# Kernel tuning notes

Hardware: AMD Instinct MI355X
Metric: run time of the kernel (lower is better)

Reference implementation:

```python
import jax, jax.numpy as jnp
import numpy as np

# Grid / filter configuration (matches init_kwargs)
NLAT_IN, NLON_IN = 361, 720
NLAT_OUT, NLON_OUT = 361, 720
K = 9                       # kernel_size for piecewise-linear basis, kernel_shape=[3,4]
PSCALE = NLON_IN // NLON_OUT  # longitude stride between output longitudes
NNZ = 65536
B, CIN, COUT = 2, 64, 64


def setup_inputs() -> dict:
    key = jax.random.key(0)
    k0, k1, k2, k3, k4, k5 = jax.random.split(key, 6)
    x = jax.random.normal(k0, (B, CIN, NLAT_IN, NLON_IN), dtype=jnp.float32)
    psi_ker_idx = jax.random.randint(k1, (NNZ,), 0, K)
    psi_row_idx = jax.random.randint(k2, (NNZ,), 0, NLAT_OUT)
    psi_col_idx = jax.random.randint(k3, (NNZ,), 0, NLAT_IN * NLON_IN)
    # quadrature-merged, normalized basis values are small positive numbers
    psi_vals = jax.random.uniform(k4, (NNZ,), dtype=jnp.float32) / K
    scale = (1.0 / (CIN * K)) ** 0.5
    weight = scale * jax.random.normal(k5, (COUT, CIN, K), dtype=jnp.float32)
    bias = jnp.zeros((COUT,), dtype=jnp.float32)
    return {
        "x": x,
        "psi_vals": psi_vals,
        "weight": weight,
        "bias": bias,
        "psi_ker_idx": psi_ker_idx,
        "psi_row_idx": psi_row_idx,
        "psi_col_idx": psi_col_idx,
    }


def reference(x, psi_vals, weight, bias, psi_ker_idx, psi_row_idx, psi_col_idx):
    """DISCO S2 conv: y[b,c,k,lo,p] = sum_nz psi_vals * x[b,c,lat_in, (lon_in+p*PSCALE)%NLON_IN]
    restricted to nz with ker==k, row==lo; then channel mixing with weight (COUT,CIN,K) + bias.
    Matches torch fallback which rolls x by PSCALE per output longitude and does sparse bmm."""
    b, c, nlat_in, nlon_in = x.shape
    lat_in = psi_col_idx // nlon_in          # (nnz,)
    lon_in = psi_col_idx % nlon_in           # (nnz,)
    seg = psi_ker_idx * NLAT_OUT + psi_row_idx  # (nnz,) segment id over (K, nlat_out)
    xf = x.reshape(b * c, nlat_in, nlon_in)

    def step(carry, p):
        lon = (lon_in + p * PSCALE) % nlon_in        # rolled longitude index, (nnz,)
        g = xf[:, lat_in, lon]                       # (BC, nnz) gather
        contrib = (psi_vals * g).T                   # (nnz, BC)
        yk = jax.ops.segment_sum(contrib, seg, num_segments=K * NLAT_OUT)  # (K*nlat_out, BC)
        y = yk.reshape(K, NLAT_OUT, b, c)
        o = jnp.einsum("klbc,ock->bol", y, weight)   # (B, COUT, nlat_out)
        return carry, o

    _, ys = jax.lax.scan(step, None, jnp.arange(NLON_OUT))  # (nlon_out, B, COUT, nlat_out)
    out = jnp.moveaxis(ys, 0, -1)                            # (B, COUT, nlat_out, nlon_out)
    return out + bias[None, :, None, None]
```

## Files before the change

### kernel.cpp

```cpp
#include <hip/hip_runtime.h>

typedef unsigned int uint;
typedef unsigned short ushort;

#define NLAT 361
#define NLON 720
#define NNZT 65536
#define CIN 64
#define COUT 64
#define NK 9
#define PADL 784
#define ROWCAP 384
#define CKTOT 576
#define YPS 168
#define WTS 640
#define XROWB (16*PADL*8)

typedef __attribute__((ext_vector_type(8))) short short8v;
typedef __attribute__((ext_vector_type(4))) float f32x4;

__device__ __forceinline__ float bfu(uint u){ return __uint_as_float(u<<16); }
__device__ __forceinline__ float bfh(uint u){ return __uint_as_float(u & 0xffff0000u); }
__device__ __forceinline__ ushort f2bf(float f){
  uint b = __float_as_uint(f);
  return (ushort)((b + 0x7fffu + ((b>>16)&1u)) >> 16);
}
__device__ __forceinline__ uint packbf2(float f0, float f1){
  uint b0 = __float_as_uint(f0), b1 = __float_as_uint(f1);
  uint r0 = (b0 + 0x7fffu + ((b0>>16)&1u)) >> 16;
  uint r1 = ((b1 + 0x7fffu + ((b1>>16)&1u)) >> 16) << 16;
  return r0 | r1;
}

__global__ __launch_bounds__(256) void k_csr(const int* __restrict__ ker, const int* __restrict__ row,
                                             const int* __restrict__ col, const float* __restrict__ vals,
                                             int2* __restrict__ meta_g, int* __restrict__ kptr_g){
  const int lo = blockIdx.x, tid = threadIdx.x;
  __shared__ int cnt2[256*NK];
  #pragma unroll
  for (int kk=0;kk<NK;kk++) cnt2[tid*NK+kk]=0;
  __syncthreads();
  for (int i=tid;i<NNZT;i+=256) if (row[i]==lo) cnt2[tid*NK + ker[i]]++;
  __syncthreads();
  if (tid==0){
    int run=0;
    for (int kk=0;kk<NK;kk++){
      kptr_g[lo*10+kk]=run;
      for (int t=0;t<256;t++){ int tmp=cnt2[t*NK+kk]; cnt2[t*NK+kk]=run; run+=tmp; }
    }
    kptr_g[lo*10+9]=run;
  }
  __syncthreads();
  for (int i=tid;i<NNZT;i+=256) if (row[i]==lo){
    int kk=ker[i];
    int off=cnt2[tid*NK+kk]++;
    if (off<ROWCAP){
      int c=col[i];
      int lat=c/NLON, lon=c-lat*NLON;
      uint vb = __float_as_uint(vals[i]) & 0xfffffc00u;
      meta_g[lo*ROWCAP+off]=make_int2(lat*XROWB + lon*8, (int)(vb | (uint)lon));
    }
  }
}

__global__ __launch_bounds__(256) void k_xb(const float* __restrict__ x, ushort* __restrict__ xb){
  const int bid=blockIdx.x, tid=threadIdx.x;
  const int b=bid/NLAT, lat=bid-b*NLAT;
  const float* xs = x + (size_t)b*CIN*NLAT*NLON + (size_t)lat*NLON;
  ushort* xd = xb + (size_t)(b*NLAT+lat)*16*PADL*4;
  const size_t S=(size_t)NLAT*NLON;
  for (int idx=tid; idx<16*PADL; idx+=256){
    int cq=idx/PADL, j=idx-cq*PADL;
    int jj = (j<NLON)? j : j-NLON;
    const float* xc = xs + (size_t)(cq*4)*S + jj;
    uint lo32 = packbf2(xc[0], xc[S]);
    uint hi32 = packbf2(xc[2*S], xc[3*S]);
    *(uint2*)(xd + (size_t)(cq*PADL + j)*4) = make_uint2(lo32, hi32);
  }
}

__global__ __launch_bounds__(256) void k_wt(const float* __restrict__ w, ushort* __restrict__ wt){
  int idx = blockIdx.x*256 + threadIdx.x;
  if (idx >= COUT*WTS) return;
  int oc = idx/WTS, ckl = idx-oc*WTS;
  int chunk = ckl/160, q = ckl-chunk*160;
  ushort v = 0;
  if (q < 144){
    int wvq=q/36, r=q-wvq*36;
    int kk=r>>2, j=r&3;
    v = f2bf(w[oc*CKTOT + (chunk*16 + wvq*4 + j)*NK + kk]);
  }
  wt[oc*WTS + ckl] = v;
}

template<int USE_XB>
__global__ __launch_bounds__(256,4) void k_main(const float* __restrict__ x, const ushort* __restrict__ xb,
    const int2* __restrict__ meta_g, const int* __restrict__ kptr_g,
    const ushort* __restrict__ wt, const float* __restrict__ bias, float* __restrict__ out){
  const int bid=blockIdx.x, tid=threadIdx.x;
  const int lo=bid/6; const int rem=bid-lo*6;
  const int b=rem/3, pq=rem-(rem/3)*3;

  __shared__ int2 meta[ROWCAP];
  __shared__ __align__(16) ushort Yp[64*YPS];

  int kp[10];
  #pragma unroll
  for (int kk=0;kk<10;kk++){ int v=kptr_g[lo*10+kk]; kp[kk]=v<ROWCAP?v:ROWCAP; }
  for (int i=tid;i<kp[9];i+=256) meta[i]=meta_g[lo*ROWCAP+i];
  for (int idx=tid; idx<64*8; idx+=256){
    int p=idx>>3, j=idx&7;
    *(uint*)((char*)Yp + p*(YPS*2) + 288 + j*4) = 0;
  }
  __syncthreads();

  const int lane=tid&63, wv=tid>>6;
  const int wvu = __builtin_amdgcn_readfirstlane(wv);
  const int l15=lane&15, kg=lane>>4;
  const char* xb8 = (const char*)xb + (size_t)b*NLAT*(size_t)XROWB;
  const char* wtb = (const char*)wt + ((wv*16+l15)*WTS + kg*8)*2;
  const char* ypb = (const char*)Yp + l15*(YPS*2) + kg*16;
  char* ydst = (char*)Yp + lane*(YPS*2) + wv*72;

  float b4[4];
  #pragma unroll
  for (int r=0;r<4;r++) b4[r]=bias[wv*16 + kg*4 + r];

#define GADDR(M) ((uint)(M).x + lanep8 + (((((uint)(M).y)&0x3ffu) >= thr) ? (uint)-5760 : 0u))
#define GVAL(M)  __uint_as_float(((uint)(M).y) & 0xfffffc00u)
#define GCONS(U,V,ACC,AI) { ACC[0][AI]+=(V)*bfu((U).x); ACC[1][AI]+=(V)*bfh((U).x); \
                            ACC[2][AI]+=(V)*bfu((U).y); ACC[3][AI]+=(V)*bfh((U).y); }
#define GB1F(M,ACC,AI) { \
      uint lon=((uint)(M).y)&0x3ffu; float v=GVAL(M); \
      int lat=(int)(((uint)(M).x)/(uint)XROWB); \
      int s=(int)lon+p0; s=(s>=NLON)?s-NLON:s; \
      int widx=s+lane; widx=(widx>=NLON)?widx-NLON:widx; \
      int base=((b*CIN + chunk*16 + wv*4)*NLAT + lat)*NLON + widx; \
      ACC[0][AI]+=v*x[base]; ACC[1][AI]+=v*x[base+NLAT*NLON]; \
      ACC[2][AI]+=v*x[base+2*NLAT*NLON]; ACC[3][AI]+=v*x[base+3*NLAT*NLON]; }

#define GSEG(ACC,KI,AI) { \
      int i=kp[KI]; const int e=kp[(KI)+1]; \
      if (USE_XB){ \
        for (; i+7<e; i+=8){ \
          int2 m0=meta[i],m1=meta[i+1],m2=meta[i+2],m3=meta[i+3]; \
          int2 m4=meta[i+4],m5=meta[i+5],m6=meta[i+6],m7=meta[i+7]; \
          uint2 u0=*(const uint2*)(xbase+GADDR(m0)); uint2 u1=*(const uint2*)(xbase+GADDR(m1)); \
          uint2 u2=*(const uint2*)(xbase+GADDR(m2)); uint2 u3=*(const uint2*)(xbase+GADDR(m3)); \
          uint2 u4=*(const uint2*)(xbase+GADDR(m4)); uint2 u5=*(const uint2*)(xbase+GADDR(m5)); \
          uint2 u6=*(const uint2*)(xbase+GADDR(m6)); uint2 u7=*(const uint2*)(xbase+GADDR(m7)); \
          GCONS(u0,GVAL(m0),ACC,AI); GCONS(u1,GVAL(m1),ACC,AI); \
          GCONS(u2,GVAL(m2),ACC,AI); GCONS(u3,GVAL(m3),ACC,AI); \
          GCONS(u4,GVAL(m4),ACC,AI); GCONS(u5,GVAL(m5),ACC,AI); \
          GCONS(u6,GVAL(m6),ACC,AI); GCONS(u7,GVAL(m7),ACC,AI); \
        } \
        for (; i+3<e; i+=4){ \
          int2 m0=meta[i],m1=meta[i+1],m2=meta[i+2],m3=meta[i+3]; \
          uint2 u0=*(const uint2*)(xbase+GADDR(m0)); uint2 u1=*(const uint2*)(xbase+GADDR(m1)); \
          uint2 u2=*(const uint2*)(xbase+GADDR(m2)); uint2 u3=*(const uint2*)(xbase+GADDR(m3)); \
          GCONS(u0,GVAL(m0),ACC,AI); GCONS(u1,GVAL(m1),ACC,AI); \
          GCONS(u2,GVAL(m2),ACC,AI); GCONS(u3,GVAL(m3),ACC,AI); \
        } \
        for (; i<e; i++){ int2 m0=meta[i]; \
          uint2 u0=*(const uint2*)(xbase+GADDR(m0)); GCONS(u0,GVAL(m0),ACC,AI); } \
      } else { \
        for (; i<e; i++){ int2 m0=meta[i]; GB1F(m0,ACC,AI); } \
      } }

  for (int pt=0;pt<4;pt++){
    const int p0 = pq*240 + pt*64;
    const uint thr = (uint)(NLON - p0);
    const uint lanep8 = (uint)(lane + p0)*8u;
    f32x4 outacc[4];
    #pragma unroll
    for (int c2=0;c2<4;c2++) outacc[c2]=(f32x4)0.f;

    for (int chunk=0;chunk<4;chunk++){
      short8v af[5];
      #pragma unroll
      for (int ks=0;ks<5;ks++)
        af[ks] = *(const short8v*)(wtb + (chunk*160 + ks*32)*2);

      const char* xbase = xb8 + (size_t)(chunk*4+wvu)*(PADL*8);

      {
        float acc1[4][5];
        #pragma unroll
        for (int j=0;j<4;j++)
          #pragma unroll
          for (int kk=0;kk<5;kk++) acc1[j][kk]=0.f;
        GSEG(acc1,0,0) GSEG(acc1,1,1) GSEG(acc1,2,2) GSEG(acc1,3,3) GSEG(acc1,4,4)
        __syncthreads();
        #pragma unroll
        for (int kk=0;kk<5;kk++){
          *(uint*)(ydst + (kk*4+0)*2) = packbf2(acc1[0][kk], acc1[1][kk]);
          *(uint*)(ydst + (kk*4+2)*2) = packbf2(acc1[2][kk], acc1[3][kk]);
        }
      }
      {
        float acc2[4][4];
        #pragma unroll
        for (int j=0;j<4;j++)
          #pragma unroll
          for (int kk=0;kk<4;kk++) acc2[j][kk]=0.f;
        GSEG(acc2,5,0) GSEG(acc2,6,1) GSEG(acc2,7,2) GSEG(acc2,8,3)
        #pragma unroll
        for (int kk=0;kk<4;kk++){
          *(uint*)(ydst + ((kk+5)*4+0)*2) = packbf2(acc2[0][kk], acc2[1][kk]);
          *(uint*)(ydst + ((kk+5)*4+2)*2) = packbf2(acc2[2][kk], acc2[3][kk]);
        }
      }
      __syncthreads();
      #pragma unroll
      for (int ptile=0;ptile<4;ptile++){
        #pragma unroll
        for (int ks=0;ks<5;ks++){
          short8v bf = *(const short8v*)(ypb + ptile*(16*YPS*2) + ks*64);
          outacc[ptile] = __builtin_amdgcn_mfma_f32_16x16x32_bf16(af[ks], bf, outacc[ptile], 0, 0, 0);
        }
      }
    }
    #pragma unroll
    for (int ptile=0;ptile<4;ptile++){
      const int pidx = pt*64 + ptile*16;
      if (pidx < 240){
        #pragma unroll
        for (int r=0;r<4;r++){
          int oc = wv*16 + kg*4 + r;
          int p  = pq*240 + pidx + l15;
          out[((size_t)(b*COUT+oc)*NLAT + lo)*NLON + p] = outacc[ptile][r] + b4[r];
        }
      }
    }
  }
}

extern "C" void kernel_launch(void* const* d_in, const int* in_sizes, int n_in,
                              void* d_out, int out_size, void* d_ws, size_t ws_size,
                              hipStream_t stream){
  const float* x   =(const float*)d_in[0];
  const float* vals=(const float*)d_in[1];
  const float* w   =(const float*)d_in[2];
  const float* bias=(const float*)d_in[3];
  const int* ker=(const int*)d_in[4];
  const int* row=(const int*)d_in[5];
  const int* col=(const int*)d_in[6];
  float* out=(float*)d_out;

  const size_t META_B=(size_t)NLAT*ROWCAP*sizeof(int2);
  const size_t KPTR_B=((size_t)NLAT*10*sizeof(int)+15)&~(size_t)15;
  const size_t WT_B=((size_t)COUT*WTS*sizeof(ushort)+15)&~(size_t)15;
  const size_t XB_B=(size_t)2*NLAT*16*PADL*4*sizeof(ushort);
  int2* meta_g=(int2*)d_ws;
  int*  kptr_g=(int*)((char*)d_ws+META_B);
  ushort* wt=(ushort*)((char*)d_ws+META_B+KPTR_B);
  ushort* xb=(ushort*)((char*)d_ws+META_B+KPTR_B+WT_B);
  const bool use_xb = ws_size >= META_B+KPTR_B+WT_B+XB_B;

  k_csr<<<dim3(NLAT), dim3(256), 0, stream>>>(ker,row,col,vals,meta_g,kptr_g);
  k_wt <<<dim3((COUT*WTS+255)/256), dim3(256), 0, stream>>>(w, wt);
  if (use_xb){
    k_xb<<<dim3(2*NLAT), dim3(256), 0, stream>>>(x, xb);
    k_main<1><<<dim3(NLAT*6), dim3(256), 0, stream>>>(x,xb,meta_g,kptr_g,wt,bias,out);
  } else {
    k_main<0><<<dim3(NLAT*6), dim3(256), 0, stream>>>(x,xb,meta_g,kptr_g,wt,bias,out);
  }
}
```

Baseline: 2.256 ms.

## Swap chunk/pt loop order, remap blocks per XCD, mask idle lanes in last tile

Loop order changes to chunk outer and pt inner. Each wave then reuses the same 4-channel slice of the bf16 x buffer across all four longitude tiles while it is cache-hot, keeping 16 MFMA accumulators live. The block index is remapped so consecutive logical blocks (same output latitude) land on the same XCD, for L2 locality of the shared meta/x rows. Lanes beyond the 240 longitudes in the last tile skip their gathers. The costs are higher register pressure from 64 accumulator floats with launch bounds of 4 blocks per CU, and weight fragments reloaded from global per MFMA.

```diff
diff --git a/kernel.cpp b/kernel.cpp
--- a/kernel.cpp
+++ b/kernel.cpp
@@ -97,7 +97,11 @@
 __global__ __launch_bounds__(256,4) void k_main(const float* __restrict__ x, const ushort* __restrict__ xb,
     const int2* __restrict__ meta_g, const int* __restrict__ kptr_g,
     const ushort* __restrict__ wt, const float* __restrict__ bias, float* __restrict__ out){
-  const int bid=blockIdx.x, tid=threadIdx.x;
+  const int nwg = NLAT*6;
+  const int qq = nwg/8, rr = nwg%8;
+  const int xcd = blockIdx.x & 7, sidx = blockIdx.x >> 3;
+  const int bid = (xcd<rr ? xcd*(qq+1) : rr*(qq+1) + (xcd-rr)*qq) + sidx;
+  const int tid=threadIdx.x;
   const int lo=bid/6; const int rem=bid-lo*6;
   const int b=rem/3, pq=rem-(rem/3)*3;
 
@@ -121,10 +125,6 @@
   const char* wtb = (const char*)wt + ((wv*16+l15)*WTS + kg*8)*2;
   const char* ypb = (const char*)Yp + l15*(YPS*2) + kg*16;
   char* ydst = (char*)Yp + lane*(YPS*2) + wv*72;
-
-  float b4[4];
-  #pragma unroll
-  for (int r=0;r<4;r++) b4[r]=bias[wv*16 + kg*4 + r];
 
 #define GADDR(M) ((uint)(M).x + lanep8 + (((((uint)(M).y)&0x3ffu) >= thr) ? (uint)-5760 : 0u))
 #define GVAL(M)  __uint_as_float(((uint)(M).y) & 0xfffffc00u)
@@ -167,21 +167,20 @@
         for (; i<e; i++){ int2 m0=meta[i]; GB1F(m0,ACC,AI); } \
       } }
 
-  for (int pt=0;pt<4;pt++){
-    const int p0 = pq*240 + pt*64;
-    const uint thr = (uint)(NLON - p0);
-    const uint lanep8 = (uint)(lane + p0)*8u;
-    f32x4 outacc[4];
+  f32x4 outacc[4][4];
+  #pragma unroll
+  for (int a=0;a<4;a++)
     #pragma unroll
-    for (int c2=0;c2<4;c2++) outacc[c2]=(f32x4)0.f;
-
-    for (int chunk=0;chunk<4;chunk++){
-      short8v af[5];
-      #pragma unroll
-      for (int ks=0;ks<5;ks++)
-        af[ks] = *(const short8v*)(wtb + (chunk*160 + ks*32)*2);
-
-      const char* xbase = xb8 + (size_t)(chunk*4+wvu)*(PADL*8);
+    for (int c2=0;c2<4;c2++) outacc[a][c2]=(f32x4)0.f;
+
+  for (int chunk=0;chunk<4;chunk++){
+    const char* xbase = xb8 + (size_t)(chunk*4+wvu)*(PADL*8);
+    #pragma unroll
+    for (int pt=0;pt<4;pt++){
+      const int p0 = pq*240 + pt*64;
+      const uint thr = (uint)(NLON - p0);
+      const uint lanep8 = (uint)(lane + p0)*8u;
+      const bool act = (pt<3) || (lane<48);
 
       {
         float acc1[4][5];
@@ -189,12 +188,14 @@
         for (int j=0;j<4;j++)
           #pragma unroll
           for (int kk=0;kk<5;kk++) acc1[j][kk]=0.f;
-        GSEG(acc1,0,0) GSEG(acc1,1,1) GSEG(acc1,2,2) GSEG(acc1,3,3) GSEG(acc1,4,4)
+        if (act){ GSEG(acc1,0,0) GSEG(acc1,1,1) GSEG(acc1,2,2) GSEG(acc1,3,3) GSEG(acc1,4,4) }
         __syncthreads();
-        #pragma unroll
-        for (int kk=0;kk<5;kk++){
-          *(uint*)(ydst + (kk*4+0)*2) = packbf2(acc1[0][kk], acc1[1][kk]);
-          *(uint*)(ydst + (kk*4+2)*2) = packbf2(acc1[2][kk], acc1[3][kk]);
+        if (act){
+          #pragma unroll
+          for (int kk=0;kk<5;kk++){
+            *(uint*)(ydst + (kk*4+0)*2) = packbf2(acc1[0][kk], acc1[1][kk]);
+            *(uint*)(ydst + (kk*4+2)*2) = packbf2(acc1[2][kk], acc1[3][kk]);
+          }
         }
       }
       {
@@ -203,11 +204,13 @@
         for (int j=0;j<4;j++)
           #pragma unroll
           for (int kk=0;kk<4;kk++) acc2[j][kk]=0.f;
-        GSEG(acc2,5,0) GSEG(acc2,6,1) GSEG(acc2,7,2) GSEG(acc2,8,3)
-        #pragma unroll
-        for (int kk=0;kk<4;kk++){
-          *(uint*)(ydst + ((kk+5)*4+0)*2) = packbf2(acc2[0][kk], acc2[1][kk]);
-          *(uint*)(ydst + ((kk+5)*4+2)*2) = packbf2(acc2[2][kk], acc2[3][kk]);
+        if (act){
+          GSEG(acc2,5,0) GSEG(acc2,6,1) GSEG(acc2,7,2) GSEG(acc2,8,3)
+          #pragma unroll
+          for (int kk=0;kk<4;kk++){
+            *(uint*)(ydst + ((kk+5)*4+0)*2) = packbf2(acc2[0][kk], acc2[1][kk]);
+            *(uint*)(ydst + ((kk+5)*4+2)*2) = packbf2(acc2[2][kk], acc2[3][kk]);
+          }
         }
       }
       __syncthreads();
@@ -216,10 +219,14 @@
         #pragma unroll
         for (int ks=0;ks<5;ks++){
           short8v bf = *(const short8v*)(ypb + ptile*(16*YPS*2) + ks*64);
-          outacc[ptile] = __builtin_amdgcn_mfma_f32_16x16x32_bf16(af[ks], bf, outacc[ptile], 0, 0, 0);
-        }
-      }
-    }
+          short8v afk = *(const short8v*)(wtb + (chunk*160 + ks*32)*2);
+          outacc[pt][ptile] = __builtin_amdgcn_mfma_f32_16x16x32_bf16(afk, bf, outacc[pt][ptile], 0, 0, 0);
+        }
+      }
+    }
+  }
+  #pragma unroll
+  for (int pt=0;pt<4;pt++)
     #pragma unroll
     for (int ptile=0;ptile<4;ptile++){
       const int pidx = pt*64 + ptile*16;
@@ -228,11 +235,10 @@
         for (int r=0;r<4;r++){
           int oc = wv*16 + kg*4 + r;
           int p  = pq*240 + pidx + l15;
-          out[((size_t)(b*COUT+oc)*NLAT + lo)*NLON + p] = outacc[ptile][r] + b4[r];
-        }
-      }
-    }
-  }
+          out[((size_t)(b*COUT+oc)*NLAT + lo)*NLON + p] = outacc[pt][ptile][r] + bias[oc];
+        }
+      }
+    }
 }
 
 extern "C" void kernel_launch(void* const* d_in, const int* in_sizes, int n_in,
```

Result: faster. 2.127 ms (-5.7%).

## Sort row nonzeros by gather address and dispatch kernel index per entry

Applied to the files above, without the earlier changes.

The CSR build no longer buckets nonzeros by kernel index. It packs the kernel index into the metadata word and rank-sorts each row's entries by gather address, so consecutive gathers touch nearby memory. The main loop then walks one flat list and uses a wave-uniform switch to pick the accumulator. It also skips gathers for inactive lanes in the last partial tile and reloads weight fragments per MFMA instead of holding them in registers. The switch per entry and the 9-wide accumulator add branching and register pressure, and the mantissa of the stored value is truncated further to make room for the index.

```diff
diff --git a/kernel.cpp b/kernel.cpp
--- a/kernel.cpp
+++ b/kernel.cpp
@@ -36,31 +36,35 @@
                                              const int* __restrict__ col, const float* __restrict__ vals,
                                              int2* __restrict__ meta_g, int* __restrict__ kptr_g){
   const int lo = blockIdx.x, tid = threadIdx.x;
-  __shared__ int cnt2[256*NK];
-  #pragma unroll
-  for (int kk=0;kk<NK;kk++) cnt2[tid*NK+kk]=0;
-  __syncthreads();
-  for (int i=tid;i<NNZT;i+=256) if (row[i]==lo) cnt2[tid*NK + ker[i]]++;
-  __syncthreads();
-  if (tid==0){
-    int run=0;
-    for (int kk=0;kk<NK;kk++){
-      kptr_g[lo*10+kk]=run;
-      for (int t=0;t<256;t++){ int tmp=cnt2[t*NK+kk]; cnt2[t*NK+kk]=run; run+=tmp; }
-    }
-    kptr_g[lo*10+9]=run;
-  }
-  __syncthreads();
+  __shared__ int cnt[256];
+  __shared__ int2 list[ROWCAP];
+  __shared__ int ntot;
+  int c=0;
+  for (int i=tid;i<NNZT;i+=256) if (row[i]==lo) c++;
+  cnt[tid]=c;
+  __syncthreads();
+  if (tid==0){ int run=0; for (int t=0;t<256;t++){ int tmp=cnt[t]; cnt[t]=run; run+=tmp; } ntot=run; }
+  __syncthreads();
+  int off=cnt[tid];
   for (int i=tid;i<NNZT;i+=256) if (row[i]==lo){
-    int kk=ker[i];
-    int off=cnt2[tid*NK+kk]++;
     if (off<ROWCAP){
-      int c=col[i];
-      int lat=c/NLON, lon=c-lat*NLON;
-      uint vb = __float_as_uint(vals[i]) & 0xfffffc00u;
-      meta_g[lo*ROWCAP+off]=make_int2(lat*XROWB + lon*8, (int)(vb | (uint)lon));
-    }
-  }
+      int cc=col[i]; int lat=cc/NLON, lon=cc-lat*NLON;
+      uint vb=__float_as_uint(vals[i])&0xffffc000u;
+      list[off]=make_int2(lat*XROWB+lon*8, (int)(vb|((uint)ker[i]<<10)|(uint)lon));
+    }
+    off++;
+  }
+  __syncthreads();
+  int n = ntot; if (n>ROWCAP) n=ROWCAP;
+  for (int i=tid;i<n;i+=256){
+    uint xi=(uint)list[i].x; int r=0;
+    for (int j=0;j<n;j++){
+      uint xj=(uint)list[j].x;
+      r += (xj<xi) || (xj==xi && j<i);
+    }
+    meta_g[lo*ROWCAP+r]=list[i];
+  }
+  if (tid==0) kptr_g[lo]=n;
 }
 
 __global__ __launch_bounds__(256) void k_xb(const float* __restrict__ x, ushort* __restrict__ xb){
@@ -104,110 +108,92 @@
   __shared__ int2 meta[ROWCAP];
   __shared__ __align__(16) ushort Yp[64*YPS];
 
-  int kp[10];
-  #pragma unroll
-  for (int kk=0;kk<10;kk++){ int v=kptr_g[lo*10+kk]; kp[kk]=v<ROWCAP?v:ROWCAP; }
-  for (int i=tid;i<kp[9];i+=256) meta[i]=meta_g[lo*ROWCAP+i];
+  int n = kptr_g[lo]; if (n>ROWCAP) n=ROWCAP;
+  for (int i=tid;i<n;i+=256) meta[i]=meta_g[lo*ROWCAP+i];
   for (int idx=tid; idx<64*8; idx+=256){
     int p=idx>>3, j=idx&7;
-    *(uint*)((char*)Yp + p*(YPS*2) + 288 + j*4) = 0;
-  }
-  __syncthreads();
-
-  const int lane=tid&63, wv=tid>>6;
+    *(uint*)((char*)Yp + p*(YPS*2) + 288 + j*4)=0;
+  }
+  __syncthreads();
+
+  const int lane=tid&63, wv=tid>>6, l15=lane&15, kg=lane>>4;
   const int wvu = __builtin_amdgcn_readfirstlane(wv);
-  const int l15=lane&15, kg=lane>>4;
   const char* xb8 = (const char*)xb + (size_t)b*NLAT*(size_t)XROWB;
   const char* wtb = (const char*)wt + ((wv*16+l15)*WTS + kg*8)*2;
   const char* ypb = (const char*)Yp + l15*(YPS*2) + kg*16;
   char* ydst = (char*)Yp + lane*(YPS*2) + wv*72;
 
-  float b4[4];
-  #pragma unroll
-  for (int r=0;r<4;r++) b4[r]=bias[wv*16 + kg*4 + r];
-
 #define GADDR(M) ((uint)(M).x + lanep8 + (((((uint)(M).y)&0x3ffu) >= thr) ? (uint)-5760 : 0u))
-#define GVAL(M)  __uint_as_float(((uint)(M).y) & 0xfffffc00u)
-#define GCONS(U,V,ACC,AI) { ACC[0][AI]+=(V)*bfu((U).x); ACC[1][AI]+=(V)*bfh((U).x); \
-                            ACC[2][AI]+=(V)*bfu((U).y); ACC[3][AI]+=(V)*bfh((U).y); }
-#define GB1F(M,ACC,AI) { \
-      uint lon=((uint)(M).y)&0x3ffu; float v=GVAL(M); \
+#define F4(U,KK) { acc[0][KK]+=v*bfu((U).x); acc[1][KK]+=v*bfh((U).x); \
+                   acc[2][KK]+=v*bfu((U).y); acc[3][KK]+=v*bfh((U).y); }
+#define CONS(M,U) { uint ky=(uint)(M).y; float v=__uint_as_float(ky&0xffffc000u); \
+      int kks=__builtin_amdgcn_readfirstlane((int)((ky>>10)&15u)); \
+      switch(kks){ \
+        case 0: F4(U,0); break; case 1: F4(U,1); break; case 2: F4(U,2); break; \
+        case 3: F4(U,3); break; case 4: F4(U,4); break; case 5: F4(U,5); break; \
+        case 6: F4(U,6); break; case 7: F4(U,7); break; default: F4(U,8); break; } }
+#define FF4(KK) { acc[0][KK]+=v*x0; acc[1][KK]+=v*x1; acc[2][KK]+=v*x2; acc[3][KK]+=v*x3; }
+#define CONSF(M) { uint ky=(uint)(M).y; float v=__uint_as_float(ky&0xffffc000u); \
       int lat=(int)(((uint)(M).x)/(uint)XROWB); \
-      int s=(int)lon+p0; s=(s>=NLON)?s-NLON:s; \
+      int s=(int)(ky&0x3ffu)+p0; s=(s>=NLON)?s-NLON:s; \
       int widx=s+lane; widx=(widx>=NLON)?widx-NLON:widx; \
-      int base=((b*CIN + chunk*16 + wv*4)*NLAT + lat)*NLON + widx; \
-      ACC[0][AI]+=v*x[base]; ACC[1][AI]+=v*x[base+NLAT*NLON]; \
-      ACC[2][AI]+=v*x[base+2*NLAT*NLON]; ACC[3][AI]+=v*x[base+3*NLAT*NLON]; }
-
-#define GSEG(ACC,KI,AI) { \
-      int i=kp[KI]; const int e=kp[(KI)+1]; \
-      if (USE_XB){ \
-        for (; i+7<e; i+=8){ \
-          int2 m0=meta[i],m1=meta[i+1],m2=meta[i+2],m3=meta[i+3]; \
-          int2 m4=meta[i+4],m5=meta[i+5],m6=meta[i+6],m7=meta[i+7]; \
-          uint2 u0=*(const uint2*)(xbase+GADDR(m0)); uint2 u1=*(const uint2*)(xbase+GADDR(m1)); \
-          uint2 u2=*(const uint2*)(xbase+GADDR(m2)); uint2 u3=*(const uint2*)(xbase+GADDR(m3)); \
-          uint2 u4=*(const uint2*)(xbase+GADDR(m4)); uint2 u5=*(const uint2*)(xbase+GADDR(m5)); \
-          uint2 u6=*(const uint2*)(xbase+GADDR(m6)); uint2 u7=*(const uint2*)(xbase+GADDR(m7)); \
-          GCONS(u0,GVAL(m0),ACC,AI); GCONS(u1,GVAL(m1),ACC,AI); \
-          GCONS(u2,GVAL(m2),ACC,AI); GCONS(u3,GVAL(m3),ACC,AI); \
-          GCONS(u4,GVAL(m4),ACC,AI); GCONS(u5,GVAL(m5),ACC,AI); \
-          GCONS(u6,GVAL(m6),ACC,AI); GCONS(u7,GVAL(m7),ACC,AI); \
-        } \
-        for (; i+3<e; i+=4){ \
-          int2 m0=meta[i],m1=meta[i+1],m2=meta[i+2],m3=meta[i+3]; \
-          uint2 u0=*(const uint2*)(xbase+GADDR(m0)); uint2 u1=*(const uint2*)(xbase+GADDR(m1)); \
-          uint2 u2=*(const uint2*)(xbase+GADDR(m2)); uint2 u3=*(const uint2*)(xbase+GADDR(m3)); \
-          GCONS(u0,GVAL(m0),ACC,AI); GCONS(u1,GVAL(m1),ACC,AI); \
-          GCONS(u2,GVAL(m2),ACC,AI); GCONS(u3,GVAL(m3),ACC,AI); \
-        } \
-        for (; i<e; i++){ int2 m0=meta[i]; \
-          uint2 u0=*(const uint2*)(xbase+GADDR(m0)); GCONS(u0,GVAL(m0),ACC,AI); } \
-      } else { \
-        for (; i<e; i++){ int2 m0=meta[i]; GB1F(m0,ACC,AI); } \
-      } }
+      int fb=((b*CIN + chunk*16 + wv*4)*NLAT + lat)*NLON + widx; \
+      float x0=x[fb], x1=x[fb+NLAT*NLON], x2=x[fb+2*NLAT*NLON], x3=x[fb+3*NLAT*NLON]; \
+      int kks=__builtin_amdgcn_readfirstlane((int)((ky>>10)&15u)); \
+      switch(kks){ \
+        case 0: FF4(0); break; case 1: FF4(1); break; case 2: FF4(2); break; \
+        case 3: FF4(3); break; case 4: FF4(4); break; case 5: FF4(5); break; \
+        case 6: FF4(6); break; case 7: FF4(7); break; default: FF4(8); break; } }
 
   for (int pt=0;pt<4;pt++){
     const int p0 = pq*240 + pt*64;
     const uint thr = (uint)(NLON - p0);
     const uint lanep8 = (uint)(lane + p0)*8u;
+    const bool act = (pt<3) || (lane<48);
+    const int jn = act ? n : 0;
+
     f32x4 outacc[4];
     #pragma unroll
     for (int c2=0;c2<4;c2++) outacc[c2]=(f32x4)0.f;
 
     for (int chunk=0;chunk<4;chunk++){
-      short8v af[5];
+      const char* xbase = xb8 + (size_t)(chunk*4+wvu)*(PADL*8);
+      float acc[4][NK];
       #pragma unroll
-      for (int ks=0;ks<5;ks++)
-        af[ks] = *(const short8v*)(wtb + (chunk*160 + ks*32)*2);
-
-      const char* xbase = xb8 + (size_t)(chunk*4+wvu)*(PADL*8);
-
-      {
-        float acc1[4][5];
-        #pragma unroll
-        for (int j=0;j<4;j++)
-          #pragma unroll
-          for (int kk=0;kk<5;kk++) acc1[j][kk]=0.f;
-        GSEG(acc1,0,0) GSEG(acc1,1,1) GSEG(acc1,2,2) GSEG(acc1,3,3) GSEG(acc1,4,4)
-        __syncthreads();
-        #pragma unroll
-        for (int kk=0;kk<5;kk++){
-          *(uint*)(ydst + (kk*4+0)*2) = packbf2(acc1[0][kk], acc1[1][kk]);
-          *(uint*)(ydst + (kk*4+2)*2) = packbf2(acc1[2][kk], acc1[3][kk]);
-        }
-      }
-      {
-        float acc2[4][4];
-        #pragma unroll
-        for (int j=0;j<4;j++)
-          #pragma unroll
-          for (int kk=0;kk<4;kk++) acc2[j][kk]=0.f;
-        GSEG(acc2,5,0) GSEG(acc2,6,1) GSEG(acc2,7,2) GSEG(acc2,8,3)
-        #pragma unroll
-        for (int kk=0;kk<4;kk++){
-          *(uint*)(ydst + ((kk+5)*4+0)*2) = packbf2(acc2[0][kk], acc2[1][kk]);
-          *(uint*)(ydst + ((kk+5)*4+2)*2) = packbf2(acc2[2][kk], acc2[3][kk]);
+      for (int j=0;j<4;j++)
+        #pragma unroll
+        for (int kk=0;kk<NK;kk++) acc[j][kk]=0.f;
+
+      int i=0;
+      if (USE_XB){
+        for (; i+7<jn; i+=8){
+          int2 m0=meta[i],m1=meta[i+1],m2=meta[i+2],m3=meta[i+3];
+          int2 m4=meta[i+4],m5=meta[i+5],m6=meta[i+6],m7=meta[i+7];
+          uint2 u0=*(const uint2*)(xbase+GADDR(m0)); uint2 u1=*(const uint2*)(xbase+GADDR(m1));
+          uint2 u2=*(const uint2*)(xbase+GADDR(m2)); uint2 u3=*(const uint2*)(xbase+GADDR(m3));
+          uint2 u4=*(const uint2*)(xbase+GADDR(m4)); uint2 u5=*(const uint2*)(xbase+GADDR(m5));
+          uint2 u6=*(const uint2*)(xbase+GADDR(m6)); uint2 u7=*(const uint2*)(xbase+GADDR(m7));
+          CONS(m0,u0); CONS(m1,u1); CONS(m2,u2); CONS(m3,u3);
+          CONS(m4,u4); CONS(m5,u5); CONS(m6,u6); CONS(m7,u7);
+        }
+        for (; i+3<jn; i+=4){
+          int2 m0=meta[i],m1=meta[i+1],m2=meta[i+2],m3=meta[i+3];
+          uint2 u0=*(const uint2*)(xbase+GADDR(m0)); uint2 u1=*(const uint2*)(xbase+GADDR(m1));
+          uint2 u2=*(const uint2*)(xbase+GADDR(m2)); uint2 u3=*(const uint2*)(xbase+GADDR(m3));
+          CONS(m0,u0); CONS(m1,u1); CONS(m2,u2); CONS(m3,u3);
+        }
+        for (; i<jn; i++){ int2 m0=meta[i];
+          uint2 u0=*(const uint2*)(xbase+GADDR(m0)); CONS(m0,u0); }
+      } else {
+        for (; i<jn; i++){ int2 m0=meta[i]; CONSF(m0); }
+      }
+
+      __syncthreads();
+      if (act){
+        #pragma unroll
+        for (int kk=0;kk<NK;kk++){
+          *(uint*)(ydst + (kk*4+0)*2) = packbf2(acc[0][kk], acc[1][kk]);
+          *(uint*)(ydst + (kk*4+2)*2) = packbf2(acc[2][kk], acc[3][kk]);
         }
       }
       __syncthreads();
@@ -216,7 +202,8 @@
         #pragma unroll
         for (int ks=0;ks<5;ks++){
           short8v bf = *(const short8v*)(ypb + ptile*(16*YPS*2) + ks*64);
-          outacc[ptile] = __builtin_amdgcn_mfma_f32_16x16x32_bf16(af[ks], bf, outacc[ptile], 0, 0, 0);
+          short8v afk = *(const short8v*)(wtb + (chunk*160 + ks*32)*2);
+          outacc[ptile]=__builtin_amdgcn_mfma_f32_16x16x32_bf16(afk,bf,outacc[ptile],0,0,0);
         }
       }
     }
@@ -227,12 +214,17 @@
         #pragma unroll
         for (int r=0;r<4;r++){
           int oc = wv*16 + kg*4 + r;
-          int p  = pq*240 + pidx + l15;
-          out[((size_t)(b*COUT+oc)*NLAT + lo)*NLON + p] = outacc[ptile][r] + b4[r];
-        }
-      }
-    }
-  }
+          out[((size_t)(b*COUT+oc)*NLAT + lo)*NLON + pq*240 + pidx + l15]
+            = outacc[ptile][r] + bias[oc];
+        }
+      }
+    }
+  }
+#undef CONSF
+#undef FF4
+#undef CONS
+#undef F4
+#undef GADDR
 }
 
 extern "C" void kernel_launch(void* const* d_in, const int* in_sizes, int n_in,
@@ -245,10 +237,10 @@
   const int* ker=(const int*)d_in[4];
   const int* row=(const int*)d_in[5];
   const int* col=(const int*)d_in[6];
-  float* out=(float*)d_out;
+  float* outp=(float*)d_out;
 
   const size_t META_B=(size_t)NLAT*ROWCAP*sizeof(int2);
-  const size_t KPTR_B=((size_t)NLAT*10*sizeof(int)+15)&~(size_t)15;
+  const size_t KPTR_B=((size_t)NLAT*sizeof(int)+15)&~(size_t)15;
   const size_t WT_B=((size_t)COUT*WTS*sizeof(ushort)+15)&~(size_t)15;
   const size_t XB_B=(size_t)2*NLAT*16*PADL*4*sizeof(ushort);
   int2* meta_g=(int2*)d_ws;
@@ -261,8 +253,8 @@
   k_wt <<<dim3((COUT*WTS+255)/256), dim3(256), 0, stream>>>(w, wt);
   if (use_xb){
     k_xb<<<dim3(2*NLAT), dim3(256), 0, stream>>>(x, xb);
-    k_main<1><<<dim3(NLAT*6), dim3(256), 0, stream>>>(x,xb,meta_g,kptr_g,wt,bias,out);
+    k_main<1><<<dim3(NLAT*6), dim3(256), 0, stream>>>(x,xb,meta_g,kptr_g,wt,bias,outp);
   } else {
-    k_main<0><<<dim3(NLAT*6), dim3(256), 0, stream>>>(x,xb,meta_g,kptr_g,wt,bias,out);
-  }
-}
+    k_main<0><<<dim3(NLAT*6), dim3(256), 0, stream>>>(x,xb,meta_g,kptr_g,wt,bias,outp);
+  }
+}
```

Result: slower. 2.602 ms (+15.3%).
